# Performance work log

Hardware: AMD Instinct MI355X
Metric: run time of the kernel (lower is better)

The kernel has to match this reference:

```python
import jax, jax.numpy as jnp
import numpy as np

D_MODEL = 1024
NUM_NEURONS = 2048
BATCH = 64
LUT_SIZE = 4096


def setup_inputs() -> dict:
    key = jax.random.key(0)
    ks = jax.random.split(key, 6)
    x = jax.random.normal(ks[0], (BATCH, D_MODEL), dtype=jnp.float32)
    t = jax.random.uniform(ks[1], (BATCH,), dtype=jnp.float32)
    W = jax.random.normal(ks[2], (NUM_NEURONS, D_MODEL), dtype=jnp.float32) * 0.02
    B_p = jnp.zeros((NUM_NEURONS, D_MODEL), dtype=jnp.float32)
    # xavier_uniform with gain=0.5 for Linear(num_neurons -> d_model), weight shape (d_model, num_neurons)
    limit = 0.5 * np.sqrt(6.0 / (NUM_NEURONS + D_MODEL))
    proj_real_w = jax.random.uniform(ks[3], (D_MODEL, NUM_NEURONS), minval=-limit, maxval=limit, dtype=jnp.float32)
    proj_imag_w = jax.random.uniform(ks[4], (D_MODEL, NUM_NEURONS), minval=-limit, maxval=limit, dtype=jnp.float32)
    # sin/cos lookup tables over [0, 2pi)
    grid = jnp.arange(LUT_SIZE, dtype=jnp.float32) * (2.0 * np.pi / LUT_SIZE)
    sin_table = jnp.sin(grid)
    cos_table = jnp.cos(grid)
    return {"x": x, "t": t, "W": W, "B_p": B_p,
            "proj_real_w": proj_real_w, "proj_imag_w": proj_imag_w,
            "sin_table": sin_table, "cos_table": cos_table}


def _lut_sin_cos(theta, sin_table, cos_table):
    # LUT lookup with linear interpolation, period 2*pi
    L = sin_table.shape[0]
    pos = theta * (np.float32(L) / np.float32(2.0 * np.pi))
    base = jnp.floor(pos)
    frac = pos - base                      # in [0, 1)
    i0 = jnp.mod(base.astype(jnp.int32), L)
    i1 = jnp.mod(i0 + 1, L)
    s = sin_table[i0] * (1.0 - frac) + sin_table[i1] * frac
    c = cos_table[i0] * (1.0 - frac) + cos_table[i1] * frac
    return s, c


def reference(x, t, W, B_p, proj_real_w, proj_imag_w, sin_table, cos_table):
    # theta: (B, N, D)
    wavelength = 1.0 + jnp.abs(W)                       # (N, D)
    theta = x[:, None, :] / wavelength + B_p + t[:, None, None]
    sin_theta, cos_theta = _lut_sin_cos(theta, sin_table, cos_table)
    cos_sum = cos_theta.sum(axis=-1)                    # (B, N)
    sin_sum = sin_theta.sum(axis=-1)                    # (B, N)
    out = cos_sum @ proj_real_w.T + sin_sum @ proj_imag_w.T  # (B, D)
    return jax.nn.silu(out)
```

## Files before the change

### kernel.cpp

```cpp
#include <hip/hip_runtime.h>
#include <math.h>

#define INV2PI 0.15915494309189535f

__global__ __launch_bounds__(256, 2) void k_sums(
    const float* __restrict__ x, const float* __restrict__ t,
    const float* __restrict__ W, const float* __restrict__ Bp,
    float2* __restrict__ S2)
{
    __shared__ float x_s[64][129];
    __shared__ float iw_s[4][128];
    __shared__ float bp_s[4][128];

    const int tid  = threadIdx.x;
    const int lane = tid & 63;
    const int wid  = __builtin_amdgcn_readfirstlane(tid >> 6);
    const int nb   = blockIdx.x * 4;

    float accC = 0.0f, accS = 0.0f;

    const float4* x4 = reinterpret_cast<const float4*>(x);

    for (int c = 0; c < 8; ++c) {
        const int d0 = c * 128;

        #pragma unroll
        for (int i = 0; i < 8; ++i) {
            int f4 = tid + 256 * i;
            int b  = f4 >> 5;
            int dq = f4 & 31;
            float4 v = x4[b * 256 + (d0 >> 2) + dq];
            x_s[b][dq * 4 + 0] = v.x;
            x_s[b][dq * 4 + 1] = v.y;
            x_s[b][dq * 4 + 2] = v.z;
            x_s[b][dq * 4 + 3] = v.w;
        }

        {
            int nl  = tid >> 6;
            int dd2 = lane * 2;
            const float2* W2 = reinterpret_cast<const float2*>(W  + (size_t)(nb + nl) * 1024 + d0);
            const float2* B2 = reinterpret_cast<const float2*>(Bp + (size_t)(nb + nl) * 1024 + d0);
            float2 w2 = W2[lane];
            float2 b2 = B2[lane];
            iw_s[nl][dd2]     = INV2PI / (1.0f + fabsf(w2.x));
            iw_s[nl][dd2 + 1] = INV2PI / (1.0f + fabsf(w2.y));
            bp_s[nl][dd2]     = b2.x * INV2PI;
            bp_s[nl][dd2 + 1] = b2.y * INV2PI;
        }
        __syncthreads();

        #pragma unroll 8
        for (int dd = 0; dd < 128; ++dd) {
            float xv = x_s[lane][dd];
            float a  = fmaf(xv, iw_s[wid][dd], bp_s[wid][dd]);
            float r  = __builtin_amdgcn_fractf(a);
            accC += __builtin_amdgcn_cosf(r);
            accS += __builtin_amdgcn_sinf(r);
        }
        __syncthreads();
    }

    const float tv = t[lane];
    const float ct = cosf(tv), st = sinf(tv);
    const int n = nb + wid;
    S2[n * 64 + lane] = make_float2(ct * accC - st * accS,
                                    st * accC + ct * accS);
}

__global__ __launch_bounds__(256, 4) void k_gemm(
    const float2* __restrict__ S2, const float* __restrict__ Pr,
    const float* __restrict__ Pi, float* __restrict__ partial)
{
    const int lane = threadIdx.x & 63;
    const int wid  = __builtin_amdgcn_readfirstlane(threadIdx.x >> 6);
    const int d0   = blockIdx.x * 16 + wid * 4;
    const int k0   = blockIdx.y * 256;

    const float* pr = Pr + (size_t)d0 * 2048 + k0;
    const float* pi = Pi + (size_t)d0 * 2048 + k0;

    float a0 = 0.f, a1 = 0.f, a2 = 0.f, a3 = 0.f;

    for (int kk = 0; kk < 256; kk += 4) {
        float2 cs[4];
        #pragma unroll
        for (int i = 0; i < 4; ++i)
            cs[i] = S2[(size_t)(k0 + kk + i) * 64 + lane];
        #pragma unroll
        for (int i = 0; i < 4; ++i) {
            a0 += pr[kk + i]        * cs[i].x + pi[kk + i]        * cs[i].y;
            a1 += pr[2048 + kk + i] * cs[i].x + pi[2048 + kk + i] * cs[i].y;
            a2 += pr[4096 + kk + i] * cs[i].x + pi[4096 + kk + i] * cs[i].y;
            a3 += pr[6144 + kk + i] * cs[i].x + pi[6144 + kk + i] * cs[i].y;
        }
    }

    float* p = partial + ((size_t)blockIdx.y * 1024 + d0) * 64 + lane;
    p[0]   = a0;
    p[64]  = a1;
    p[128] = a2;
    p[192] = a3;
}

__global__ __launch_bounds__(256, 4) void k_reduce_silu(
    const float* __restrict__ partial, float* __restrict__ out)
{
    __shared__ float T[64][65];
    const int lane = threadIdx.x & 63;
    const int rr   = threadIdx.x >> 6;
    const int dt   = blockIdx.x * 64;

    #pragma unroll
    for (int i = 0; i < 16; ++i) {
        int dd = rr + 4 * i;
        float s = 0.f;
        #pragma unroll
        for (int ss = 0; ss < 8; ++ss)
            s += partial[((size_t)ss * 1024 + dt + dd) * 64 + lane];
        float sig = 1.0f / (1.0f + __expf(-s));
        T[dd][lane] = s * sig;
    }
    __syncthreads();
    #pragma unroll
    for (int i = 0; i < 16; ++i) {
        int b = rr + 4 * i;
        out[(size_t)b * 1024 + dt + lane] = T[lane][b];
    }
}

extern "C" void kernel_launch(void* const* d_in, const int* in_sizes, int n_in,
                              void* d_out, int out_size, void* d_ws, size_t ws_size,
                              hipStream_t stream)
{
    const float* x  = (const float*)d_in[0];
    const float* t  = (const float*)d_in[1];
    const float* W  = (const float*)d_in[2];
    const float* Bp = (const float*)d_in[3];
    const float* Pr = (const float*)d_in[4];
    const float* Pi = (const float*)d_in[5];

    float*  out     = (float*)d_out;
    float2* S2      = (float2*)d_ws;
    float*  partial = (float*)((char*)d_ws + (1 << 20));

    k_sums<<<512, 256, 0, stream>>>(x, t, W, Bp, S2);
    k_gemm<<<dim3(64, 8), 256, 0, stream>>>(S2, Pr, Pi, partial);
    k_reduce_silu<<<16, 256, 0, stream>>>(partial, out);
}
```

Baseline: 165.4 us.

## Remap k_sums so lanes span d with per-batch register accumulators

The sums kernel now puts the d_model dimension across lanes, using float4 loads of W and B_p, and keeps 32 per-batch accumulators in registers. A block holds 512 threads, with two wave groups each covering half the batch. This removes the per-chunk shared-memory staging of the inverse wavelength and B_p values and cuts redundant LDS reads, but the per-lane partial sums then have to be reduced through an XOR-swizzled shared-memory transpose. The reduce+SiLU kernel is flattened to one output element per thread over more blocks, dropping its LDS transpose in exchange for strided reads of the partial buffer. The larger register and LDS footprint (64 KB of shared memory per block) may limit occupancy.

Result: slower. 229.5 us (+38.8%).

```diff
diff --git a/kernel.cpp b/kernel.cpp
--- a/kernel.cpp
+++ b/kernel.cpp
@@ -3,69 +3,98 @@
 
 #define INV2PI 0.15915494309189535f
 
-__global__ __launch_bounds__(256, 2) void k_sums(
+__global__ __launch_bounds__(512, 4) void k_sums(
     const float* __restrict__ x, const float* __restrict__ t,
     const float* __restrict__ W, const float* __restrict__ Bp,
     float2* __restrict__ S2)
 {
-    __shared__ float x_s[64][129];
-    __shared__ float iw_s[4][128];
-    __shared__ float bp_s[4][128];
+    __shared__ float x_s[64 * 256];
 
     const int tid  = threadIdx.x;
     const int lane = tid & 63;
     const int wid  = __builtin_amdgcn_readfirstlane(tid >> 6);
-    const int nb   = blockIdx.x * 4;
+    const int nl   = wid & 3;
+    const int bh   = wid >> 2;
+    const int n    = blockIdx.x * 4 + nl;
 
-    float accC = 0.0f, accS = 0.0f;
+    float accC[32], accS[32];
+    #pragma unroll
+    for (int j = 0; j < 32; ++j) { accC[j] = 0.f; accS[j] = 0.f; }
 
     const float4* x4 = reinterpret_cast<const float4*>(x);
 
-    for (int c = 0; c < 8; ++c) {
-        const int d0 = c * 128;
+    for (int c = 0; c < 4; ++c) {
+        __syncthreads();
 
         #pragma unroll
-        for (int i = 0; i < 8; ++i) {
-            int f4 = tid + 256 * i;
-            int b  = f4 >> 5;
-            int dq = f4 & 31;
-            float4 v = x4[b * 256 + (d0 >> 2) + dq];
-            x_s[b][dq * 4 + 0] = v.x;
-            x_s[b][dq * 4 + 1] = v.y;
-            x_s[b][dq * 4 + 2] = v.z;
-            x_s[b][dq * 4 + 3] = v.w;
+        for (int i = 0; i < 32; ++i) {
+            int f4 = i * 512 + tid;
+            int b  = f4 >> 6;
+            int dq = f4 & 63;
+            float4 v = x4[b * 256 + c * 64 + dq];
+            *reinterpret_cast<float4*>(&x_s[f4 << 2]) = v;
         }
 
-        {
-            int nl  = tid >> 6;
-            int dd2 = lane * 2;
-            const float2* W2 = reinterpret_cast<const float2*>(W  + (size_t)(nb + nl) * 1024 + d0);
-            const float2* B2 = reinterpret_cast<const float2*>(Bp + (size_t)(nb + nl) * 1024 + d0);
-            float2 w2 = W2[lane];
-            float2 b2 = B2[lane];
-            iw_s[nl][dd2]     = INV2PI / (1.0f + fabsf(w2.x));
-            iw_s[nl][dd2 + 1] = INV2PI / (1.0f + fabsf(w2.y));
-            bp_s[nl][dd2]     = b2.x * INV2PI;
-            bp_s[nl][dd2 + 1] = b2.y * INV2PI;
-        }
+        float4 w4 = *reinterpret_cast<const float4*>(W  + (size_t)n * 1024 + c * 256 + 4 * lane);
+        float4 b4 = *reinterpret_cast<const float4*>(Bp + (size_t)n * 1024 + c * 256 + 4 * lane);
+        float4 iw, bp;
+        iw.x = INV2PI / (1.f + fabsf(w4.x));
+        iw.y = INV2PI / (1.f + fabsf(w4.y));
+        iw.z = INV2PI / (1.f + fabsf(w4.z));
+        iw.w = INV2PI / (1.f + fabsf(w4.w));
+        bp.x = b4.x * INV2PI;
+        bp.y = b4.y * INV2PI;
+        bp.z = b4.z * INV2PI;
+        bp.w = b4.w * INV2PI;
+
         __syncthreads();
 
-        #pragma unroll 8
-        for (int dd = 0; dd < 128; ++dd) {
-            float xv = x_s[lane][dd];
-            float a  = fmaf(xv, iw_s[wid][dd], bp_s[wid][dd]);
-            float r  = __builtin_amdgcn_fractf(a);
-            accC += __builtin_amdgcn_cosf(r);
-            accS += __builtin_amdgcn_sinf(r);
+        #pragma unroll
+        for (int j = 0; j < 32; ++j) {
+            const float4 xv = *reinterpret_cast<const float4*>(
+                &x_s[(bh * 32 + j) * 256 + 4 * lane]);
+            float a, r;
+            a = fmaf(xv.x, iw.x, bp.x); r = __builtin_amdgcn_fractf(a);
+            accC[j] += __builtin_amdgcn_cosf(r);
+            accS[j] += __builtin_amdgcn_sinf(r);
+            a = fmaf(xv.y, iw.y, bp.y); r = __builtin_amdgcn_fractf(a);
+            accC[j] += __builtin_amdgcn_cosf(r);
+            accS[j] += __builtin_amdgcn_sinf(r);
+            a = fmaf(xv.z, iw.z, bp.z); r = __builtin_amdgcn_fractf(a);
+            accC[j] += __builtin_amdgcn_cosf(r);
+            accS[j] += __builtin_amdgcn_sinf(r);
+            a = fmaf(xv.w, iw.w, bp.w); r = __builtin_amdgcn_fractf(a);
+            accC[j] += __builtin_amdgcn_cosf(r);
+            accS[j] += __builtin_amdgcn_sinf(r);
         }
-        __syncthreads();
     }
 
-    const float tv = t[lane];
-    const float ct = cosf(tv), st = sinf(tv);
-    const int n = nb + wid;
-    S2[n * 64 + lane] = make_float2(ct * accC - st * accS,
-                                    st * accC + ct * accS);
+    __syncthreads();
+    float* sl = x_s + (wid << 11);
+    const int bm = lane & 31;
+    const int kb = (lane >> 5) << 5;
+
+    #pragma unroll
+    for (int j = 0; j < 32; ++j) sl[j * 64 + (lane ^ j)] = accC[j];
+    float sumC = 0.f;
+    #pragma unroll
+    for (int k = 0; k < 32; ++k) sumC += sl[bm * 64 + ((kb + k) ^ bm)];
+    #pragma unroll
+    for (int j = 0; j < 32; ++j) sl[j * 64 + (lane ^ j)] = accS[j];
+    float sumS = 0.f;
+    #pragma unroll
+    for (int k = 0; k < 32; ++k) sumS += sl[bm * 64 + ((kb + k) ^ bm)];
+
+    sumC += __shfl_xor(sumC, 32);
+    sumS += __shfl_xor(sumS, 32);
+
+    if (lane < 32) {
+        const int b  = bh * 32 + lane;
+        const float tv = t[b];
+        const float ct = cosf(tv), st = sinf(tv);
+        S2[n * 64 + b] = make_float2(ct * sumC - st * sumS,
+                                     st * sumC + ct * sumS);
+    }
 }
 
 __global__ __launch_bounds__(256, 4) void k_gemm(
@@ -106,27 +135,18 @@
 __global__ __launch_bounds__(256, 4) void k_reduce_silu(
     const float* __restrict__ partial, float* __restrict__ out)
 {
-    __shared__ float T[64][65];
     const int lane = threadIdx.x & 63;
-    const int rr   = threadIdx.x >> 6;
-    const int dt   = blockIdx.x * 64;
+    const int gw   = blockIdx.x * 4 + (threadIdx.x >> 6);
+    const int b    = gw >> 4;
+    const int d    = ((gw & 15) << 6) + lane;
 
+    float s = 0.f;
     #pragma unroll
-    for (int i = 0; i < 16; ++i) {
-        int dd = rr + 4 * i;
-        float s = 0.f;
-        #pragma unroll
-        for (int ss = 0; ss < 8; ++ss)
-            s += partial[((size_t)ss * 1024 + dt + dd) * 64 + lane];
-        float sig = 1.0f / (1.0f + __expf(-s));
-        T[dd][lane] = s * sig;
-    }
-    __syncthreads();
-    #pragma unroll
-    for (int i = 0; i < 16; ++i) {
-        int b = rr + 4 * i;
-        out[(size_t)b * 1024 + dt + lane] = T[lane][b];
-    }
+    for (int ss = 0; ss < 8; ++ss)
+        s += partial[((size_t)ss * 1024 + d) * 64 + b];
+
+    float sig = 1.0f / (1.0f + __expf(-s));
+    out[(size_t)b * 1024 + d] = s * sig;
 }
 
 extern "C" void kernel_launch(void* const* d_in, const int* in_sizes, int n_in,
@@ -144,7 +164,7 @@
     float2* S2      = (float2*)d_ws;
     float*  partial = (float*)((char*)d_ws + (1 << 20));
 
-    k_sums<<<512, 256, 0, stream>>>(x, t, W, Bp, S2);
+    k_sums<<<512, 512, 0, stream>>>(x, t, W, Bp, S2);
     k_gemm<<<dim3(64, 8), 256, 0, stream>>>(S2, Pr, Pi, partial);
-    k_reduce_silu<<<16, 256, 0, stream>>>(partial, out);
+    k_reduce_silu<<<256, 256, 0, stream>>>(partial, out);
 }
```
